# Performance work log

Hardware: AMD Instinct MI355X
Metric: run time of the kernel (lower is better)

Reference implementation:

```python
import jax, jax.numpy as jnp
import numpy as np

B, T, DIM, H, HD = 2, 2048, 1024, 16, 64
ROPE_THETA = 500000.0
EPS = 1e-6
SOFTCAP = 50.0


def _rmsnorm(x, gamma):
    # x: (..., HD)
    rms = jax.lax.rsqrt(jnp.mean(x * x, axis=-1, keepdims=True) + EPS)
    return x * rms * gamma


def _apply_rope(x, cos, sin):
    # x: (B, T, H, HD); cos/sin: (T, HD//2). Pairs are interleaved (even, odd).
    xe = x[..., 0::2]
    xo = x[..., 1::2]
    c = cos[None, :, None, :]
    s = sin[None, :, None, :]
    re = xe * c - xo * s
    im = xe * s + xo * c
    # re-interleave: (..., HD//2, 2) -> (..., HD)
    return jnp.stack([re, im], axis=-1).reshape(x.shape)


def setup_inputs() -> dict:
    key = jax.random.key(0)
    kx, kq, kk, kv, ko = jax.random.split(key, 5)
    x = jax.random.normal(kx, (B, T, DIM), dtype=jnp.float32)
    sc = 0.02
    wq = jax.random.normal(kq, (H * HD, DIM), dtype=jnp.float32) * sc
    wk = jax.random.normal(kk, (HD, DIM), dtype=jnp.float32) * sc
    wv = jax.random.normal(kv, (HD, DIM), dtype=jnp.float32) * sc
    wo = jax.random.normal(ko, (DIM, H * HD), dtype=jnp.float32) * sc
    q_gamma = jnp.ones((HD,), dtype=jnp.float32)
    k_gamma = jnp.ones((HD,), dtype=jnp.float32)
    # RoPE tables (same as torch.polar precompute)
    inv_freq = 1.0 / (ROPE_THETA ** (np.arange(0, HD, 2, dtype=np.float32) / HD))
    t = np.arange(T, dtype=np.float32)
    ang = np.outer(t, inv_freq)  # (T, HD//2)
    freqs_cos = jnp.asarray(np.cos(ang), dtype=jnp.float32)
    freqs_sin = jnp.asarray(np.sin(ang), dtype=jnp.float32)
    # causal additive mask (T, T)
    causal = np.tril(np.ones((T, T), dtype=bool))
    mask = jnp.asarray(np.where(causal, 0.0, -1e9).astype(np.float32))
    return {"x": x, "wq": wq, "wk": wk, "wv": wv, "wo": wo,
            "q_gamma": q_gamma, "k_gamma": k_gamma,
            "freqs_cos": freqs_cos, "freqs_sin": freqs_sin, "mask": mask}


def reference(x, wq, wk, wv, wo, q_gamma, k_gamma, freqs_cos, freqs_sin, mask):
    b, t, _ = x.shape
    q = (x @ wq.T).reshape(b, t, H, HD)            # (B,T,H,HD)
    k = (x @ wk.T).reshape(b, t, 1, HD)            # (B,T,1,HD) single KV head
    v = x @ wv.T                                    # (B,T,HD)
    q = _rmsnorm(q, q_gamma)
    k = _rmsnorm(k, k_gamma)
    q = _apply_rope(q, freqs_cos, freqs_sin)
    k = _apply_rope(k, freqs_cos, freqs_sin)[:, :, 0, :]  # (B,S,HD)
    scale = HD ** -0.5
    # MQA: single K/V head shared across H query heads
    attn = jnp.einsum('bthd,bsd->bhts', q, k) * scale      # (B,H,T,S)
    attn = jnp.tanh(attn / SOFTCAP) * SOFTCAP
    attn = attn + mask[None, None, :, :]
    p = jax.nn.softmax(attn, axis=-1)
    out = jnp.einsum('bhts,bsd->bthd', p, v).reshape(b, t, H * HD)
    return out @ wo.T
```

## Files before the change

### kernel.cpp

```cpp
#include <hip/hip_runtime.h>
#include <hip/hip_bf16.h>
#include <stdint.h>
#include <math.h>

#define B_ 2
#define T_ 2048
#define DIM_ 1024
#define H_ 16
#define HD_ 64
#define NROWS_ (B_*T_)
#define NQKV 1152
#define UNITS_PER_BH 80
#define NUNITS (16 * UNITS_PER_BH)
#define CT_SCALE 0.18033688f
#define C2_ (-6.40603e-5f)
#define C4_ (4.92447e-9f)

typedef __bf16 bf16_t;
typedef __attribute__((ext_vector_type(8))) __bf16 bf16x8;
typedef __attribute__((ext_vector_type(4))) __bf16 bf16x4;
typedef __attribute__((ext_vector_type(4))) float f32x4;
typedef __attribute__((ext_vector_type(16))) float f32x16;

__device__ __forceinline__ float wave_sum64(float v) {
#pragma unroll
  for (int off = 32; off > 0; off >>= 1) v += __shfl_xor(v, off, 64);
  return v;
}

__device__ __forceinline__ int cb(int q) {
  int a = q >> 3, r = q & 7;
  return 4 * a * (a + 1) + r * (a + 1);
}

__device__ __forceinline__ bf16_t* swz(bf16_t* base, int row, int col) {
  return (bf16_t*)((char*)base + (row << 7) + (((col << 1) ^ ((row & 7) << 4))));
}

__device__ __forceinline__ f32x16 mfma32(bf16x8 a, bf16x8 b, f32x16 c) {
  return __builtin_amdgcn_mfma_f32_32x32x16_bf16(a, b, c, 0, 0, 0);
}

__device__ __forceinline__ unsigned cvt_pk(float lo, float hi) {
  unsigned r;
  asm("v_cvt_pk_bf16_f32 %0, %1, %2" : "=v"(r) : "v"(lo), "v"(hi));
  return r;
}
__device__ __forceinline__ void plswap(unsigned& x, unsigned& y) {
  asm volatile("v_permlane32_swap_b32 %0, %1" : "+v"(x), "+v"(y));
}

#define C_S0 (NROWS_*DIM_/8)
#define C_S1 (C_S0 + DIM_*DIM_/8)
#define C_S2 (C_S1 + HD_*DIM_/8)
#define C_S3 (C_S2 + HD_*DIM_/8)
#define C_S4 (C_S3 + DIM_*DIM_/8)
__global__ __launch_bounds__(256) void cvt_all(
    const float* __restrict__ x, const float* __restrict__ wq,
    const float* __restrict__ wk, const float* __restrict__ wv,
    const float* __restrict__ wo, bf16_t* __restrict__ xb,
    bf16_t* __restrict__ wqkvb, bf16_t* __restrict__ wob) {
  int i = blockIdx.x * 256 + threadIdx.x;
  if (i >= C_S4) return;
  const float* src; bf16_t* dst; int j;
  if (i < C_S0)      { src = x;  dst = xb; j = i; }
  else if (i < C_S1) { src = wq; dst = wqkvb; j = i - C_S0; }
  else if (i < C_S2) { src = wk; dst = wqkvb + (size_t)DIM_ * DIM_; j = i - C_S1; }
  else if (i < C_S3) { src = wv; dst = wqkvb + (size_t)(DIM_ + HD_) * DIM_; j = i - C_S2; }
  else               { src = wo; dst = wob; j = i - C_S3; }
  float4 a = ((const float4*)src)[2 * (size_t)j];
  float4 b = ((const float4*)src)[2 * (size_t)j + 1];
  bf16x8 o;
  o[0] = (bf16_t)a.x; o[1] = (bf16_t)a.y; o[2] = (bf16_t)a.z; o[3] = (bf16_t)a.w;
  o[4] = (bf16_t)b.x; o[5] = (bf16_t)b.y; o[6] = (bf16_t)b.z; o[7] = (bf16_t)b.w;
  *(bf16x8*)(dst + 8 * (size_t)j) = o;
}

template<int OUTF32, int QKV>
__global__ __launch_bounds__(256) void gemm_bt(const bf16_t* __restrict__ A,
    const bf16_t* __restrict__ Bw, void* __restrict__ Cv,
    bf16_t* __restrict__ vt, int N, int K) {
  __shared__ bf16_t As[2][128 * 32];
  __shared__ bf16_t Bs[2][64 * 32];
  const int tid = threadIdx.x;
  const int w = tid >> 6, lane = tid & 63;
  const int row0 = blockIdx.x * 128, col0 = blockIdx.y * 64;
  const int wm = w >> 1, wn = w & 1;
  const int rr = lane & 15, kg = lane >> 4;
  f32x4 acc[4][2];
#pragma unroll
  for (int i = 0; i < 4; ++i)
#pragma unroll
    for (int j = 0; j < 2; ++j) acc[i][j] = (f32x4){0.f, 0.f, 0.f, 0.f};
  const int srow = lane >> 2;
  const int skoff = ((lane & 3) ^ (srow & 3)) << 3;
  for (int kt = 0; kt < K; kt += 64) {
    __syncthreads();
#pragma unroll
    for (int kk = 0; kk < 2; ++kk) {
#pragma unroll
      for (int c = 0; c < 2; ++c) {
        const int chunk = 2 * w + c;
        const bf16_t* sA =
            A + (size_t)(row0 + chunk * 16 + srow) * K + kt + 32 * kk + skoff;
        __builtin_amdgcn_global_load_lds(
            (const __attribute__((address_space(1))) unsigned int*)(uintptr_t)sA,
            (__attribute__((address_space(3))) unsigned int*)(uintptr_t)(&As[kk][chunk * 512]),
            16, 0, 0);
      }
      const bf16_t* sB =
          Bw + (size_t)(col0 + w * 16 + srow) * K + kt + 32 * kk + skoff;
      __builtin_amdgcn_global_load_lds(
          (const __attribute__((address_space(1))) unsigned int*)(uintptr_t)sB,
          (__attribute__((address_space(3))) unsigned int*)(uintptr_t)(&Bs[kk][w * 512]),
          16, 0, 0);
    }
    __syncthreads();
#pragma unroll
    for (int kk = 0; kk < 2; ++kk) {
      bf16x8 af[4], bfv[2];
#pragma unroll
      for (int mi = 0; mi < 4; ++mi) {
        int r = 64 * wm + 16 * mi + rr;
        af[mi] = *(const bf16x8*)(&As[kk][r * 32 + ((kg ^ (r & 3)) << 3)]);
      }
#pragma unroll
      for (int ni = 0; ni < 2; ++ni) {
        int r = 32 * wn + 16 * ni + rr;
        bfv[ni] = *(const bf16x8*)(&Bs[kk][r * 32 + ((kg ^ (r & 3)) << 3)]);
      }
#pragma unroll
      for (int mi = 0; mi < 4; ++mi)
#pragma unroll
        for (int ni = 0; ni < 2; ++ni)
          acc[mi][ni] = __builtin_amdgcn_mfma_f32_16x16x32_bf16(af[mi], bfv[ni],
                                                                acc[mi][ni], 0, 0, 0);
    }
  }
  const int crow = (lane >> 4) * 4, ccol = lane & 15;
  if (QKV && col0 == DIM_ + HD_) {
#pragma unroll
    for (int mi = 0; mi < 4; ++mi)
#pragma unroll
      for (int ni = 0; ni < 2; ++ni) {
        int d = 32 * wn + 16 * ni + ccol;
        size_t rg = (size_t)(row0 + 64 * wm + 16 * mi + crow);
        bf16x4 pk;
#pragma unroll
        for (int r = 0; r < 4; ++r) pk[r] = (bf16_t)acc[mi][ni][r];
        *(bf16x4*)(vt + (size_t)d * NROWS_ + rg) = pk;
      }
  } else {
#pragma unroll
    for (int mi = 0; mi < 4; ++mi)
#pragma unroll
      for (int ni = 0; ni < 2; ++ni)
#pragma unroll
        for (int r = 0; r < 4; ++r) {
          size_t rg = (size_t)(row0 + 64 * wm + 16 * mi + crow + r);
          size_t cg = (size_t)(col0 + 32 * wn + 16 * ni + ccol);
          if (OUTF32) ((float*)Cv)[rg * N + cg] = acc[mi][ni][r];
          else        ((bf16_t*)Cv)[rg * N + cg] = (bf16_t)acc[mi][ni][r];
        }
  }
}

__global__ __launch_bounds__(512) void normrope(bf16_t* __restrict__ qkv,
    const float* __restrict__ qg, const float* __restrict__ kgm,
    const float* __restrict__ fc, const float* __restrict__ fs) {
  const int row = blockIdx.x;
  const int w = threadIdx.x >> 6, d = threadIdx.x & 63;
  const int t = row & (T_ - 1);
  const float c = fc[t * (HD_ / 2) + (d >> 1)];
  const float s = fs[t * (HD_ / 2) + (d >> 1)];
  for (int hh = w; hh <= H_; hh += 8) {
    bf16_t* ptr = qkv + (size_t)row * NQKV + hh * HD_;
    float g = (hh < H_) ? qg[d] : kgm[d];
    float val = (float)ptr[d];
    float ssum = wave_sum64(val * val);
    float rms = rsqrtf(ssum * (1.f / HD_) + 1e-6f);
    val *= rms * g;
    float partner = __shfl_xor(val, 1, 64);
    float res = ((d & 1) == 0) ? (val * c - partner * s) : (partner * s + val * c);
    if (hh < H_) res *= CT_SCALE;
    ptr[d] = (bf16_t)res;
  }
}

__global__ __launch_bounds__(512, 4) void attn_part(const bf16_t* __restrict__ qkv,
                                                    const bf16_t* __restrict__ vt,
                                                    bf16_t* __restrict__ partO,
                                                    float* __restrict__ partL) {
  __shared__ __align__(16) char SMEM[32768];
  __shared__ float Lx[4][32];
  bf16_t* Ks = (bf16_t*)SMEM;
  bf16_t* Vt = (bf16_t*)(SMEM + 16384);
  const int tid = threadIdx.x;
  const int w = tid >> 6, lane = tid & 63;
  const int u = NUNITS - 1 - (int)blockIdx.x;
  const int bh = u / UNITS_PER_BH;
  const int rem = u - bh * UNITS_PER_BH;
  const int b = bh >> 3, hp = bh & 7;
  int qt = 0;
  while (qt < 31 && cb(qt + 1) <= rem) ++qt;
  const int chunk = rem - cb(qt);
  const int nt = min(8, qt + 1 - chunk * 8);
  const int NP = (nt + 1) >> 1;
  const int qt0 = qt * 64;
  const int h0 = hp * 2;
  const size_t bT = (size_t)b * T_;
  const int lo = lane & 31, hi = lane >> 5;
  const int hw = w >> 2, qg = (w >> 1) & 1, ks = w & 1, g2 = w >> 1;

  bf16x8 qf[4];
  {
    const bf16_t* qbase =
        qkv + (bT + qt0 + 32 * qg + lo) * NQKV + (h0 + hw) * HD_ + hi * 8;
#pragma unroll
    for (int s = 0; s < 4; ++s) qf[s] = *(const bf16x8*)(qbase + 16 * s);
  }
  const int srow = tid >> 3, scol = (tid & 7) * 8;
  const bf16_t* kp = qkv + (bT + chunk * 512 + srow) * NQKV + DIM_ + scol;
  const bf16_t* vtp = vt + (size_t)srow * NROWS_ + bT + chunk * 512 + scol;
  uint4 kpre0, kpre1, vpre0, vpre1;

#define PREFETCH() do {                                                       \
    kpre0 = *(const uint4*)kp;                                                \
    kpre1 = *(const uint4*)(kp + (size_t)64 * NQKV);                          \
    vpre0 = *(const uint4*)vtp;                                               \
    vpre1 = *(const uint4*)(vtp + 64);                                        \
    kp += (size_t)128 * NQKV;                                                 \
    vtp += 128;                                                               \
  } while (0)
#define STAGE() do {                                                          \
    *(uint4*)swz(Ks, srow, scol) = kpre0;                                     \
    *(uint4*)swz(Ks + 4096, srow, scol) = kpre1;                              \
    *(uint4*)swz(Vt, srow, scol) = vpre0;                                     \
    *(uint4*)swz(Vt + 4096, srow, scol) = vpre1;                              \
  } while (0)

  f32x16 accO0 = {}, accO1 = {};
  float l_ = 0.f;
  bf16_t* KsP = Ks + ks * 4096;
  bf16_t* VtP = Vt + ks * 4096;

  PREFETCH();
  STAGE();
  if (NP > 1) PREFETCH();
  __syncthreads();

  for (int j = 0; j < NP; ++j) {
    const int ctl = 2 * j + ks;
    if (ctl < nt) {
      const int ct = chunk * 8 + ctl;
      f32x16 S0 = {}, S1 = {};
      __builtin_amdgcn_s_setprio(1);
#pragma unroll
      for (int s = 0; s < 4; ++s) {
        bf16x8 kf0 = *(const bf16x8*)swz(KsP, lo, 16 * s + hi * 8);
        bf16x8 kf1 = *(const bf16x8*)swz(KsP, 32 + lo, 16 * s + hi * 8);
        S0 = mfma32(kf0, qf[s], S0);
        S1 = mfma32(kf1, qf[s], S1);
      }
      __builtin_amdgcn_s_setprio(0);
      const bool full = (64 * ct + 63 <= qt0 + 32 * qg);
      const int qrel = qt0 + 32 * qg + lo - 64 * ct;
      float psum = 0.f;
#pragma unroll
      for (int kh = 0; kh < 2; ++kh)
#pragma unroll
        for (int r = 0; r < 16; ++r) {
          float t = (kh == 0) ? S0[r] : S1[r];
          float t2 = t * t;
          float ww = fmaf(t2, C4_, C2_);
          float pv = exp2f(fmaf(t * t2, ww, t));
          if (!full) {
            int koff = 32 * kh + (r & 3) + 8 * (r >> 2) + 4 * hi;
            pv = (koff <= qrel) ? pv : 0.f;
          }
          psum += pv;
          if (kh == 0) S0[r] = pv; else S1[r] = pv;
        }
      psum += __shfl_xor(psum, 32, 64);
      l_ += psum;
      __builtin_amdgcn_s_setprio(1);
#pragma unroll
      for (int s = 0; s < 4; ++s) {
        const int base = (s & 1) * 8;
        float p0, p1, p2, p3, p4, p5, p6, p7;
        if (s >> 1) {
          p0 = S1[base + 0]; p1 = S1[base + 1]; p2 = S1[base + 2]; p3 = S1[base + 3];
          p4 = S1[base + 4]; p5 = S1[base + 5]; p6 = S1[base + 6]; p7 = S1[base + 7];
        } else {
          p0 = S0[base + 0]; p1 = S0[base + 1]; p2 = S0[base + 2]; p3 = S0[base + 3];
          p4 = S0[base + 4]; p5 = S0[base + 5]; p6 = S0[base + 6]; p7 = S0[base + 7];
        }
        unsigned a0 = cvt_pk(p0, p1), a1 = cvt_pk(p2, p3);
        unsigned b0 = cvt_pk(p4, p5), b1 = cvt_pk(p6, p7);
        plswap(a0, b0);
        plswap(a1, b1);
        union { unsigned uu[4]; bf16x8 v; } pa;
        pa.uu[0] = a0; pa.uu[1] = a1; pa.uu[2] = b0; pa.uu[3] = b1;
        bf16x8 vf0 = *(const bf16x8*)swz(VtP, lo, 16 * s + hi * 8);
        bf16x8 vf1 = *(const bf16x8*)swz(VtP, 32 + lo, 16 * s + hi * 8);
        accO0 = mfma32(pa.v, vf0, accO0);
        accO1 = mfma32(pa.v, vf1, accO1);
      }
      __builtin_amdgcn_s_setprio(0);
    }
    __syncthreads();
    if (j + 1 < NP) {
      STAGE();
      if (j + 2 < NP) PREFETCH();
      __syncthreads();
    }
  }
#undef PREFETCH
#undef STAGE

  float* exch = (float*)SMEM;
  float* my = exch + ((size_t)g2 * 64 + lane) * 32;
  if (ks == 1) {
#pragma unroll
    for (int qd = 0; qd < 4; ++qd) {
      int sl = (qd ^ (lane & 7)) * 4;
      f32x4 t0 = {accO0[4*qd], accO0[4*qd+1], accO0[4*qd+2], accO0[4*qd+3]};
      *(f32x4*)(my + sl) = t0;
      int sl2 = ((qd + 4) ^ (lane & 7)) * 4;
      f32x4 t1 = {accO1[4*qd], accO1[4*qd+1], accO1[4*qd+2], accO1[4*qd+3]};
      *(f32x4*)(my + sl2) = t1;
    }
    if (hi == 0) Lx[g2][lo] = l_;
  }
  __syncthreads();
  if (ks == 0) {
#pragma unroll
    for (int qd = 0; qd < 4; ++qd) {
      int sl = (qd ^ (lane & 7)) * 4;
      f32x4 t0 = *(const f32x4*)(my + sl);
      accO0[4*qd] += t0[0]; accO0[4*qd+1] += t0[1];
      accO0[4*qd+2] += t0[2]; accO0[4*qd+3] += t0[3];
      int sl2 = ((qd + 4) ^ (lane & 7)) * 4;
      f32x4 t1 = *(const f32x4*)(my + sl2);
      accO1[4*qd] += t1[0]; accO1[4*qd+1] += t1[1];
      accO1[4*qd+2] += t1[2]; accO1[4*qd+3] += t1[3];
    }
    float l_tot = l_ + Lx[g2][lo];
    bf16_t* po = partO + ((size_t)u * 2 + hw) * 4096;
#pragma unroll
    for (int rq = 0; rq < 4; ++rq)
#pragma unroll
      for (int c = 0; c < 4; ++c) {
        int q = 32 * qg + 8 * rq + 4 * hi + c;
        po[q * 64 + lo] = (bf16_t)accO0[4 * rq + c];
        po[q * 64 + 32 + lo] = (bf16_t)accO1[4 * rq + c];
      }
    if (hi == 0) partL[((size_t)u * 2 + hw) * 64 + 32 * qg + lo] = l_tot;
  }
}

__global__ __launch_bounds__(256) void attn_reduce(const bf16_t* __restrict__ partO,
                                                   const float* __restrict__ partL,
                                                   bf16_t* __restrict__ att) {
  const int qt = blockIdx.x, h = blockIdx.y, b = blockIdx.z;
  const int nch = (qt + 8) >> 3;
  const size_t ubase = (size_t)(b * 8 + (h >> 1)) * UNITS_PER_BH + cb(qt);
  const int hw = h & 1;
  const int tid = threadIdx.x;
  const int q = tid >> 2, dblk = (tid & 3) * 16;
  f32x4 o[4] = {};
  float l = 0.f;
  for (int c = 0; c < nch; ++c) {
    const bf16_t* po = partO + ((ubase + c) * 2 + hw) * 4096 + q * 64 + dblk;
    bf16x8 v0 = *(const bf16x8*)po;
    bf16x8 v1 = *(const bf16x8*)(po + 8);
#pragma unroll
    for (int i = 0; i < 4; ++i) o[0][i] += (float)v0[i];
#pragma unroll
    for (int i = 0; i < 4; ++i) o[1][i] += (float)v0[4 + i];
#pragma unroll
    for (int i = 0; i < 4; ++i) o[2][i] += (float)v1[i];
#pragma unroll
    for (int i = 0; i < 4; ++i) o[3][i] += (float)v1[4 + i];
    l += partL[((ubase + c) * 2 + hw) * 64 + q];
  }
  const float linv = 1.f / l;
  bf16_t* dst = att + ((size_t)(b * T_ + qt * 64 + q)) * DIM_ + h * HD_ + dblk;
  bf16x8 r0, r1;
#pragma unroll
  for (int i = 0; i < 4; ++i) { r0[i] = (bf16_t)(o[0][i] * linv);
                                r0[4+i] = (bf16_t)(o[1][i] * linv);
                                r1[i] = (bf16_t)(o[2][i] * linv);
                                r1[4+i] = (bf16_t)(o[3][i] * linv); }
  *(bf16x8*)dst = r0;
  *(bf16x8*)(dst + 8) = r1;
}

extern "C" void kernel_launch(void* const* d_in, const int* in_sizes, int n_in,
                              void* d_out, int out_size, void* d_ws, size_t ws_size,
                              hipStream_t stream) {
  const float* x   = (const float*)d_in[0];
  const float* wq  = (const float*)d_in[1];
  const float* wk  = (const float*)d_in[2];
  const float* wv  = (const float*)d_in[3];
  const float* wo  = (const float*)d_in[4];
  const float* qg  = (const float*)d_in[5];
  const float* kgm = (const float*)d_in[6];
  const float* fc  = (const float*)d_in[7];
  const float* fs  = (const float*)d_in[8];
  float* out = (float*)d_out;

  bf16_t* xb    = (bf16_t*)d_ws;
  bf16_t* wqkvb = xb + (size_t)NROWS_ * DIM_;
  bf16_t* wob   = wqkvb + (size_t)NQKV * DIM_;
  bf16_t* qkvo  = wob + (size_t)DIM_ * DIM_;
  bf16_t* attb  = qkvo + (size_t)NROWS_ * NQKV;
  bf16_t* partO = attb + (size_t)NROWS_ * DIM_;
  float*  partL = (float*)(partO + (size_t)NUNITS * 2 * 4096);
  bf16_t* vtb   = (bf16_t*)(partL + (size_t)NUNITS * 2 * 64);

  cvt_all<<<(C_S4 + 255) / 256, 256, 0, stream>>>(x, wq, wk, wv, wo, xb, wqkvb, wob);
  gemm_bt<0, 1><<<dim3(NROWS_ / 128, NQKV / 64), 256, 0, stream>>>(
      xb, wqkvb, qkvo, vtb, NQKV, DIM_);
  normrope<<<NROWS_, 512, 0, stream>>>(qkvo, qg, kgm, fc, fs);
  attn_part<<<NUNITS, 512, 0, stream>>>(qkvo, vtb, partO, partL);
  attn_reduce<<<dim3(T_ / 64, H_, B_), 256, 0, stream>>>(partO, partL, attb);
  gemm_bt<1, 0><<<dim3(NROWS_ / 128, DIM_ / 64), 256, 0, stream>>>(
      attb, wob, out, nullptr, DIM_, DIM_);
}
```

Before: 117.8 us.

## Fuse RMSNorm+RoPE into QKV GEMM epilogue and finalize single-chunk attention directly

Removes the separate normrope kernel by computing per-row sums of squares across the two column waves in the QKV GEMM epilogue via shuffles and shared memory, then applying RMSNorm, RoPE and the Q scale before storing. Attention query tiles with only one KV chunk (qt<8) now normalize by l and write the final output directly, and attn_reduce launches only for the remaining tiles. This drops one kernel launch and a read/write pass over the QKV buffer, plus partial-output traffic for early tiles. The cost is a heavier GEMM epilogue with an extra barrier and uncoalesced cos/sin loads.

Result: faster. 111.0 us (-5.7%).

```diff
diff --git a/kernel.cpp b/kernel.cpp
--- a/kernel.cpp
+++ b/kernel.cpp
@@ -21,12 +21,6 @@
 typedef __attribute__((ext_vector_type(4))) __bf16 bf16x4;
 typedef __attribute__((ext_vector_type(4))) float f32x4;
 typedef __attribute__((ext_vector_type(16))) float f32x16;
-
-__device__ __forceinline__ float wave_sum64(float v) {
-#pragma unroll
-  for (int off = 32; off > 0; off >>= 1) v += __shfl_xor(v, off, 64);
-  return v;
-}
 
 __device__ __forceinline__ int cb(int q) {
   int a = q >> 3, r = q & 7;
@@ -79,9 +73,12 @@
 template<int OUTF32, int QKV>
 __global__ __launch_bounds__(256) void gemm_bt(const bf16_t* __restrict__ A,
     const bf16_t* __restrict__ Bw, void* __restrict__ Cv,
-    bf16_t* __restrict__ vt, int N, int K) {
+    bf16_t* __restrict__ vt, const float* __restrict__ qg,
+    const float* __restrict__ kgm, const float* __restrict__ fc,
+    const float* __restrict__ fs, int N, int K) {
   __shared__ bf16_t As[2][128 * 32];
   __shared__ bf16_t Bs[2][64 * 32];
+  __shared__ float RowS[128][2];
   const int tid = threadIdx.x;
   const int w = tid >> 6, lane = tid & 63;
   const int row0 = blockIdx.x * 128, col0 = blockIdx.y * 64;
@@ -150,6 +147,43 @@
         for (int r = 0; r < 4; ++r) pk[r] = (bf16_t)acc[mi][ni][r];
         *(bf16x4*)(vt + (size_t)d * NROWS_ + rg) = pk;
       }
+  } else if (QKV) {
+    const float* gam = (col0 < DIM_) ? qg : kgm;
+    const float g0 = gam[32 * wn + ccol];
+    const float g1 = gam[32 * wn + 16 + ccol];
+    const float qs = (col0 < DIM_) ? CT_SCALE : 1.f;
+#pragma unroll
+    for (int mi = 0; mi < 4; ++mi)
+#pragma unroll
+      for (int r = 0; r < 4; ++r) {
+        float ss = acc[mi][0][r] * acc[mi][0][r] + acc[mi][1][r] * acc[mi][1][r];
+        ss += __shfl_xor(ss, 1, 64);
+        ss += __shfl_xor(ss, 2, 64);
+        ss += __shfl_xor(ss, 4, 64);
+        ss += __shfl_xor(ss, 8, 64);
+        if (ccol == 0) RowS[64 * wm + 16 * mi + crow + r][wn] = ss;
+      }
+    __syncthreads();
+#pragma unroll
+    for (int mi = 0; mi < 4; ++mi)
+#pragma unroll
+      for (int r = 0; r < 4; ++r) {
+        const int row = 64 * wm + 16 * mi + crow + r;
+        const int t = (row0 + row) & (T_ - 1);
+        const float rms =
+            rsqrtf((RowS[row][0] + RowS[row][1]) * (1.f / HD_) + 1e-6f);
+#pragma unroll
+        for (int ni = 0; ni < 2; ++ni) {
+          const int col = 32 * wn + 16 * ni + ccol;
+          float val = acc[mi][ni][r] * rms * (ni ? g1 : g0);
+          float partner = __shfl_xor(val, 1, 64);
+          float c = fc[t * (HD_ / 2) + (col >> 1)];
+          float s = fs[t * (HD_ / 2) + (col >> 1)];
+          float res = ((ccol & 1) == 0) ? (val * c - partner * s)
+                                        : (partner * s + val * c);
+          ((bf16_t*)Cv)[(size_t)(row0 + row) * N + col0 + col] = (bf16_t)(res * qs);
+        }
+      }
   } else {
 #pragma unroll
     for (int mi = 0; mi < 4; ++mi)
@@ -165,34 +199,14 @@
   }
 }
 
-__global__ __launch_bounds__(512) void normrope(bf16_t* __restrict__ qkv,
-    const float* __restrict__ qg, const float* __restrict__ kgm,
-    const float* __restrict__ fc, const float* __restrict__ fs) {
-  const int row = blockIdx.x;
-  const int w = threadIdx.x >> 6, d = threadIdx.x & 63;
-  const int t = row & (T_ - 1);
-  const float c = fc[t * (HD_ / 2) + (d >> 1)];
-  const float s = fs[t * (HD_ / 2) + (d >> 1)];
-  for (int hh = w; hh <= H_; hh += 8) {
-    bf16_t* ptr = qkv + (size_t)row * NQKV + hh * HD_;
-    float g = (hh < H_) ? qg[d] : kgm[d];
-    float val = (float)ptr[d];
-    float ssum = wave_sum64(val * val);
-    float rms = rsqrtf(ssum * (1.f / HD_) + 1e-6f);
-    val *= rms * g;
-    float partner = __shfl_xor(val, 1, 64);
-    float res = ((d & 1) == 0) ? (val * c - partner * s) : (partner * s + val * c);
-    if (hh < H_) res *= CT_SCALE;
-    ptr[d] = (bf16_t)res;
-  }
-}
-
 __global__ __launch_bounds__(512, 4) void attn_part(const bf16_t* __restrict__ qkv,
                                                     const bf16_t* __restrict__ vt,
                                                     bf16_t* __restrict__ partO,
-                                                    float* __restrict__ partL) {
+                                                    float* __restrict__ partL,
+                                                    bf16_t* __restrict__ att) {
   __shared__ __align__(16) char SMEM[32768];
   __shared__ float Lx[4][32];
+  __shared__ float Lf[4][32];
   bf16_t* Ks = (bf16_t*)SMEM;
   bf16_t* Vt = (bf16_t*)(SMEM + 16384);
   const int tid = threadIdx.x;
@@ -346,23 +360,40 @@
       accO1[4*qd+2] += t1[2]; accO1[4*qd+3] += t1[3];
     }
     float l_tot = l_ + Lx[g2][lo];
-    bf16_t* po = partO + ((size_t)u * 2 + hw) * 4096;
-#pragma unroll
-    for (int rq = 0; rq < 4; ++rq)
-#pragma unroll
-      for (int c = 0; c < 4; ++c) {
-        int q = 32 * qg + 8 * rq + 4 * hi + c;
-        po[q * 64 + lo] = (bf16_t)accO0[4 * rq + c];
-        po[q * 64 + 32 + lo] = (bf16_t)accO1[4 * rq + c];
-      }
-    if (hi == 0) partL[((size_t)u * 2 + hw) * 64 + 32 * qg + lo] = l_tot;
+    if (qt < 8) {
+      if (hi == 0) Lf[g2][lo] = l_tot;
+#pragma unroll
+      for (int rq = 0; rq < 4; ++rq) {
+        f32x4 lv = *(const f32x4*)&Lf[g2][8 * rq + 4 * hi];
+#pragma unroll
+        for (int c = 0; c < 4; ++c) {
+          size_t grow = bT + qt0 + 32 * qg + 8 * rq + 4 * hi + c;
+          float linv = 1.f / lv[c];
+          att[grow * DIM_ + (h0 + hw) * HD_ + lo] =
+              (bf16_t)(accO0[4 * rq + c] * linv);
+          att[grow * DIM_ + (h0 + hw) * HD_ + 32 + lo] =
+              (bf16_t)(accO1[4 * rq + c] * linv);
+        }
+      }
+    } else {
+      bf16_t* po = partO + ((size_t)u * 2 + hw) * 4096;
+#pragma unroll
+      for (int rq = 0; rq < 4; ++rq)
+#pragma unroll
+        for (int c = 0; c < 4; ++c) {
+          int q = 32 * qg + 8 * rq + 4 * hi + c;
+          po[q * 64 + lo] = (bf16_t)accO0[4 * rq + c];
+          po[q * 64 + 32 + lo] = (bf16_t)accO1[4 * rq + c];
+        }
+      if (hi == 0) partL[((size_t)u * 2 + hw) * 64 + 32 * qg + lo] = l_tot;
+    }
   }
 }
 
 __global__ __launch_bounds__(256) void attn_reduce(const bf16_t* __restrict__ partO,
                                                    const float* __restrict__ partL,
                                                    bf16_t* __restrict__ att) {
-  const int qt = blockIdx.x, h = blockIdx.y, b = blockIdx.z;
+  const int qt = blockIdx.x + 8, h = blockIdx.y, b = blockIdx.z;
   const int nch = (qt + 8) >> 3;
   const size_t ubase = (size_t)(b * 8 + (h >> 1)) * UNITS_PER_BH + cb(qt);
   const int hw = h & 1;
@@ -421,10 +452,9 @@
 
   cvt_all<<<(C_S4 + 255) / 256, 256, 0, stream>>>(x, wq, wk, wv, wo, xb, wqkvb, wob);
   gemm_bt<0, 1><<<dim3(NROWS_ / 128, NQKV / 64), 256, 0, stream>>>(
-      xb, wqkvb, qkvo, vtb, NQKV, DIM_);
-  normrope<<<NROWS_, 512, 0, stream>>>(qkvo, qg, kgm, fc, fs);
-  attn_part<<<NUNITS, 512, 0, stream>>>(qkvo, vtb, partO, partL);
-  attn_reduce<<<dim3(T_ / 64, H_, B_), 256, 0, stream>>>(partO, partL, attb);
+      xb, wqkvb, qkvo, vtb, qg, kgm, fc, fs, NQKV, DIM_);
+  attn_part<<<NUNITS, 512, 0, stream>>>(qkvo, vtb, partO, partL, attb);
+  attn_reduce<<<dim3(24, H_, B_), 256, 0, stream>>>(partO, partL, attb);
   gemm_bt<1, 0><<<dim3(NROWS_ / 128, DIM_ / 64), 256, 0, stream>>>(
-      attb, wob, out, nullptr, DIM_, DIM_);
-}
+      attb, wob, out, nullptr, nullptr, nullptr, nullptr, nullptr, DIM_, DIM_);
+}
```
